# Kernel optimization log

Measured on AMD Instinct MI355X. Metric: run time of the kernel, lower is better.

Reference implementation:

```python
import jax, jax.numpy as jnp
import numpy as np

D_MODEL = 1024
N_HEADS = 16
ORDER = 6          # P
P2 = 2 * ORDER - 1 # 11 collapsed Chebyshev terms
EPS_CLAMP = 1e-6
EPS_DEN = 1e-7


def _beta_np():
    # alpha_j = (j+1)^{-1.5}, j = 0..P-1
    j = np.arange(ORDER, dtype=np.float32)
    alpha = (j + 1.0) ** (-1.5)
    tail = np.flip(np.cumsum(np.flip(alpha)))  # tail[i] = sum_{j>=i} alpha_j
    beta = np.concatenate([np.zeros(1, np.float32), tail[1:].astype(np.float32), np.zeros(ORDER - 1, np.float32)])
    return beta / beta.sum()


def _cheb(x):
    T = [jnp.ones_like(x), x]
    for _ in range(2, P2):
        T.append(2.0 * x * T[-1] - T[-2])
    return jnp.stack(T, axis=3)


def setup_inputs() -> dict:
    key = jax.random.key(0)
    k1, k2, k3 = jax.random.split(key, 3)
    B, S, D = 2, 1024, D_MODEL
    x = jax.random.normal(k1, (B, S, D), dtype=jnp.float32)
    W_in = jax.random.normal(k2, (3 * D, D), dtype=jnp.float32) * 0.02
    W_out = jax.random.normal(k3, (D, D), dtype=jnp.float32) * 0.02
    return {"x": x, "W_in": W_in, "W_out": W_out}


def reference(x, W_in, W_out):
    B, S, D = x.shape
    H, Dh = N_HEADS, D // N_HEADS

    # fused QKV projection (Linear, no bias): y = x @ W_in^T
    qkv = jnp.einsum('bsd,ed->bse', x, W_in)
    q, k, v = jnp.split(qkv, 3, axis=-1)
    # (B,S,H,Dh) -> (B,H,S,Dh)
    q = q.reshape(B, S, H, Dh).transpose(0, 2, 1, 3)
    k = k.reshape(B, S, H, Dh).transpose(0, 2, 1, 3)
    v = v.reshape(B, S, H, Dh).transpose(0, 2, 1, 3)

    inv_sqrt_d = 1.0 / jnp.sqrt(jnp.float32(Dh))
    xq = jnp.clip(q * inv_sqrt_d, -1.0 + EPS_CLAMP, 1.0 - EPS_CLAMP)
    xk = jnp.clip(k * inv_sqrt_d, -1.0 + EPS_CLAMP, 1.0 - EPS_CLAMP)

    Tq = _cheb(xq)  # (B,H,S,P2,Dh)
    Tk = _cheb(xk)  # (B,H,S,P2,Dh)

    beta = jnp.asarray(_beta_np())  # (P2,), same for all heads (fixed buffer)

    # causal prefix sums over sequence dim
    Tv = Tk * v[:, :, :, None, :]             # (B,H,S,P2,Dh)
    kv_prefix = jnp.cumsum(Tv, axis=2)        # (B,H,S,P2,Dh)
    ks_prefix = jnp.cumsum(Tk.sum(axis=-1), axis=2)  # (B,H,S,P2)

    kv_beta = kv_prefix * beta[None, None, None, :, None]
    k_beta = ks_prefix * beta[None, None, None, :]

    num = (Tq * kv_beta).sum(axis=3)                 # (B,H,S,Dh)
    den = (Tq.sum(axis=-1) * k_beta).sum(axis=3)     # (B,H,S)   den_normalization='none'

    out_h = num / (den[..., None] + EPS_DEN)
    out = out_h.transpose(0, 2, 1, 3).reshape(B, S, H * Dh)
    return jnp.einsum('bsd,ed->bse', out, W_out)
```

## Files before the change

kernel.cpp:

```cpp
#include <hip/hip_runtime.h>
#include <hip/hip_bf16.h>
#include <cstddef>
#include <cstdint>

#define BATCH 2
#define SEQ   1024
#define DMODEL 1024
#define NHEADS 16
#define DHEAD 64
#define E3D   3072
#define NCHUNK 64
#define CHUNK 16

#define BETA1 0.45736626f
#define BETA2 0.26218724f
#define BETA3 0.15594524f
#define BETA4 0.08693904f
#define BETA5 0.03756222f

#define RSCALE 2048.f
#define RINV   4.8828125e-4f

typedef __attribute__((ext_vector_type(8))) _Float16 half8;
typedef __attribute__((ext_vector_type(16))) float floatx16;

__device__ __forceinline__ void cp16(const void* g, void* l) {
    __builtin_amdgcn_global_load_lds(
        (const __attribute__((address_space(1))) void*)(uintptr_t)g,
        (__attribute__((address_space(3))) void*)(uintptr_t)l,
        16, 0, 0);
}

__device__ __forceinline__ void split2(float x, unsigned short* H, unsigned short* M) {
    _Float16 h = (_Float16)x;
    float r = (x - (float)h) * RSCALE;
    _Float16 m = (_Float16)r;
    *H = __builtin_bit_cast(unsigned short, h);
    *M = __builtin_bit_cast(unsigned short, m);
}

__device__ __forceinline__ void split2x4(const float4 v,
                                         unsigned short* h, unsigned short* m,
                                         size_t i4) {
    float vv[4] = {v.x, v.y, v.z, v.w};
    unsigned short hh[4], mm[4];
#pragma unroll
    for (int j = 0; j < 4; j++) split2(vv[j], &hh[j], &mm[j]);
    ((ushort4*)h)[i4] = make_ushort4(hh[0], hh[1], hh[2], hh[3]);
    ((ushort4*)m)[i4] = make_ushort4(mm[0], mm[1], mm[2], mm[3]);
}

__device__ __forceinline__ void cheb5(float x, float T[6]) {
    T[0] = 1.f; T[1] = x;
    float tx2 = 2.f * x;
    T[2] = tx2 * T[1] - T[0];
    T[3] = tx2 * T[2] - T[1];
    T[4] = tx2 * T[3] - T[2];
    T[5] = tx2 * T[4] - T[3];
}

__device__ __forceinline__ float clampx(float v) {
    return fminf(fmaxf(v * 0.125f, -1.f + 1e-6f), 1.f - 1e-6f);
}

__device__ __forceinline__ float wave_sum(float x) {
#pragma unroll
    for (int m = 32; m >= 1; m >>= 1) x += __shfl_xor(x, m, 64);
    return x;
}

__global__ __launch_bounds__(256) void k_splitall(
    const float* __restrict__ x, const float* __restrict__ Win,
    unsigned short* __restrict__ Xh, unsigned short* __restrict__ Xm,
    unsigned short* __restrict__ Wh, unsigned short* __restrict__ Wm)
{
    const float* in; unsigned short *h, *m; int i;
    if (blockIdx.x < 2048) {
        in = x; h = Xh; m = Xm;
        i = blockIdx.x * 256 + threadIdx.x;
    } else {
        in = Win; h = Wh; m = Wm;
        i = (blockIdx.x - 2048) * 256 + threadIdx.x;
    }
    split2x4(((const float4*)in)[i], h, m, i);
}

template<int TN>
__global__ __launch_bounds__(256, 2) void gemm_w32(
    const unsigned short* __restrict__ Ah, const unsigned short* __restrict__ Am,
    const unsigned short* __restrict__ Bh, const unsigned short* __restrict__ Bm,
    float* __restrict__ C, int M, int N, int K)
{
    constexpr int NT  = TN / 64;
    constexpr int ASZ = 64 * 32;
    constexpr int BSZ = TN * 32;
    __shared__ unsigned short lds[2 * ASZ + 2 * BSZ];

    const int tid  = threadIdx.x;
    const int w    = tid >> 6;
    const int lane = tid & 63;
    const int m0 = blockIdx.y * 64;
    const int n0 = blockIdx.x * TN;

    const int arow = w * 16 + (lane >> 2);
    const int asg  = (lane & 3) ^ ((arow >> 1) & 3);
    const size_t offA = (size_t)(m0 + arow) * K + asg * 8;
    const int ldsA = (w * 16) * 32;
    size_t offB[NT];
    int ldsB[NT];
#pragma unroll
    for (int j = 0; j < NT; j++) {
        const int brow = j * 64 + w * 16 + (lane >> 2);
        const int bsg  = (lane & 3) ^ ((brow >> 1) & 3);
        offB[j] = (size_t)(n0 + brow) * K + bsg * 8;
        ldsB[j] = (j * 64 + w * 16) * 32;
    }

    const int l32 = lane & 31, q32 = lane >> 5;
    const int wm = w & 1, wn = w >> 1;
    const int ra = wm * 32 + l32;
    const int abase = ra * 32, aswz = (ra >> 1) & 3;
    int bbase[NT], bswz[NT];
#pragma unroll
    for (int nt = 0; nt < NT; nt++) {
        const int rb = wn * (TN / 2) + nt * 32 + l32;
        bbase[nt] = rb * 32;
        bswz[nt] = (rb >> 1) & 3;
    }

    floatx16 acc1[NT] = {};
    floatx16 acc2[NT] = {};

    for (int k0 = 0; k0 < K; k0 += 32) {
        __syncthreads();
        cp16(Ah + offA + k0, &lds[ldsA]);
        cp16(Am + offA + k0, &lds[ASZ + ldsA]);
#pragma unroll
        for (int j = 0; j < NT; j++) {
            cp16(Bh + offB[j] + k0, &lds[2 * ASZ + ldsB[j]]);
            cp16(Bm + offB[j] + k0, &lds[2 * ASZ + BSZ + ldsB[j]]);
        }
        __syncthreads();

#pragma unroll
        for (int kk = 0; kk < 2; kk++) {
            const int ksel = kk * 2 + q32;
            half8 fah = *(const half8*)&lds[abase + ((ksel ^ aswz) * 8)];
            half8 fam = *(const half8*)&lds[ASZ + abase + ((ksel ^ aswz) * 8)];
            half8 fbh[NT], fbm[NT];
#pragma unroll
            for (int nt = 0; nt < NT; nt++) {
                fbh[nt] = *(const half8*)&lds[2 * ASZ + bbase[nt] + ((ksel ^ bswz[nt]) * 8)];
                fbm[nt] = *(const half8*)&lds[2 * ASZ + BSZ + bbase[nt] + ((ksel ^ bswz[nt]) * 8)];
            }
#pragma unroll
            for (int nt = 0; nt < NT; nt++) {
                acc1[nt] = __builtin_amdgcn_mfma_f32_32x32x16_f16(fah, fbh[nt], acc1[nt], 0, 0, 0);
                acc2[nt] = __builtin_amdgcn_mfma_f32_32x32x16_f16(fah, fbm[nt], acc2[nt], 0, 0, 0);
                acc2[nt] = __builtin_amdgcn_mfma_f32_32x32x16_f16(fam, fbh[nt], acc2[nt], 0, 0, 0);
            }
        }
    }

    const int r0 = m0 + wm * 32 + q32 * 4;
#pragma unroll
    for (int nt = 0; nt < NT; nt++) {
        const int c0 = n0 + wn * (TN / 2) + nt * 32 + l32;
#pragma unroll
        for (int reg = 0; reg < 16; reg++) {
            const int row = r0 + (reg & 3) + 8 * (reg >> 2);
            C[(size_t)row * N + c0] = acc1[nt][reg] + acc2[nt][reg] * RINV;
        }
    }
}

__global__ __launch_bounds__(256) void k_mid(
    const float* __restrict__ Wout,
    unsigned short* __restrict__ Wouth, unsigned short* __restrict__ Woutm,
    const float* __restrict__ qkv,
    float* __restrict__ SQB, float* __restrict__ SK, float* __restrict__ KVC)
{
    const int blk = blockIdx.x;
    if (blk < 1024) {
        int i = blk * 256 + threadIdx.x;
        split2x4(((const float4*)Wout)[i], Wouth, Woutm, i);
        return;
    }
    if (blk < 9216) {
        const int lane = threadIdx.x & 63;
        const int pos  = (blk - 1024) * 4 + (threadIdx.x >> 6);
        const int bh = pos >> 10, s = pos & 1023;
        const int b = bh >> 4, h = bh & 15;
        const float* base = qkv + (size_t)(b * SEQ + s) * E3D + h * DHEAD + lane;
        float xq = clampx(base[0]);
        float xk = clampx(base[1024]);
        float Tq[6], Tk[6];
        cheb5(xq, Tq); cheb5(xk, Tk);
        const float BETA[5] = {BETA1, BETA2, BETA3, BETA4, BETA5};
#pragma unroll
        for (int p = 1; p <= 5; p++) {
            float sq = wave_sum(Tq[p]);
            float sk = wave_sum(Tk[p]);
            if (lane == 0) {
                SQB[(size_t)pos * 5 + p - 1] = sq * BETA[p - 1];
                SK[(size_t)pos * 5 + p - 1]  = sk;
            }
        }
        return;
    }
    {
        const int lane = threadIdx.x & 63;
        const int cid = (blk - 9216) * 4 + (threadIdx.x >> 6);
        const int bh = cid >> 6, chunk = cid & 63;
        const int b = bh >> 4, h = bh & 15;
        const float* kb = qkv + (size_t)(b * SEQ + chunk * CHUNK) * E3D + 1024 + h * DHEAD + lane;
        float kv[5] = {0.f, 0.f, 0.f, 0.f, 0.f};
#pragma unroll
        for (int i = 0; i < CHUNK; i++) {
            const float* row = kb + (size_t)i * E3D;
            float xk = clampx(row[0]);
            float v = row[1024];
            float T[6]; cheb5(xk, T);
#pragma unroll
            for (int p = 1; p <= 5; p++) kv[p - 1] += T[p] * v;
        }
#pragma unroll
        for (int p = 0; p < 5; p++) KVC[((size_t)cid * 5 + p) * 64 + lane] = kv[p];
    }
}

__global__ __launch_bounds__(320) void k_prefix(float* __restrict__ KVC,
                                                const float* __restrict__ SK,
                                                float* __restrict__ SKP)
{
    __shared__ float csum[NCHUNK * 5];
    const int bh = blockIdx.x;
    const int t = threadIdx.x;
    float v[NCHUNK];
    const size_t base = (size_t)bh * NCHUNK * 320 + t;
#pragma unroll
    for (int c = 0; c < NCHUNK; c++) v[c] = KVC[base + (size_t)c * 320];
    float run = 0.f;
#pragma unroll
    for (int c = 0; c < NCHUNK; c++) {
        KVC[base + (size_t)c * 320] = run;
        run += v[c];
    }
    {
        const int chunk = t / 5, p = t % 5;
        const float* sb = SK + ((size_t)bh * SEQ + chunk * CHUNK) * 5 + p;
        float s = 0.f;
#pragma unroll
        for (int i = 0; i < CHUNK; i++) s += sb[i * 5];
        csum[chunk * 5 + p] = s;
    }
    __syncthreads();
    if (t < 5) {
        float run2 = 0.f;
        for (int c = 0; c < NCHUNK; c++) {
            SKP[((size_t)bh * NCHUNK + c) * 5 + t] = run2;
            run2 += csum[c * 5 + t];
        }
    }
}

__global__ __launch_bounds__(256) void k_out(const float* __restrict__ qkv,
                                             const float* __restrict__ KVC,
                                             const float* __restrict__ SK,
                                             const float* __restrict__ SKP,
                                             const float* __restrict__ SQB,
                                             unsigned short* __restrict__ OH,
                                             unsigned short* __restrict__ OM)
{
    const int lane = threadIdx.x & 63;
    const int cid = blockIdx.x * 4 + (threadIdx.x >> 6);
    const int bh = cid >> 6, chunk = cid & 63;
    const int b = bh >> 4, h = bh & 15;
    const float BETA[5] = {BETA1, BETA2, BETA3, BETA4, BETA5};

    const int li = lane & 15;
    const int pos = bh * SEQ + chunk * CHUNK + li;
    float den_r = 0.f;
#pragma unroll
    for (int p = 0; p < 5; p++) {
        float v = SK[(size_t)pos * 5 + p];
#pragma unroll
        for (int off = 1; off < 16; off <<= 1) {
            float n = __shfl_up(v, off, 64);
            if (li >= off) v += n;
        }
        den_r += SQB[(size_t)pos * 5 + p] * (SKP[((size_t)bh * NCHUNK + chunk) * 5 + p] + v);
    }

    float kv[5];
#pragma unroll
    for (int p = 0; p < 5; p++) kv[p] = KVC[((size_t)cid * 5 + p) * 64 + lane];

    const float* qb = qkv + (size_t)(b * SEQ + chunk * CHUNK) * E3D + h * DHEAD + lane;
    size_t obase = (size_t)(b * SEQ + chunk * CHUNK) * DMODEL + h * DHEAD + lane;
#pragma unroll
    for (int i = 0; i < CHUNK; i++) {
        const float* row = qb + (size_t)i * E3D;
        float xq = clampx(row[0]);
        float xk = clampx(row[1024]);
        float v = row[2048];
        float Tk_[6]; cheb5(xk, Tk_);
#pragma unroll
        for (int p = 1; p <= 5; p++) kv[p - 1] += Tk_[p] * v;
        float Tq_[6]; cheb5(xq, Tq_);
        float num = 0.f;
#pragma unroll
        for (int p = 1; p <= 5; p++) num += BETA[p - 1] * Tq_[p] * kv[p - 1];
        float d = __shfl(den_r, i, 64);
        float val = num / (d + 1e-7f);
        unsigned short hh, mm;
        split2(val, &hh, &mm);
        size_t oi = obase + (size_t)i * DMODEL;
        OH[oi] = hh; OM[oi] = mm;
    }
}


extern "C" void kernel_launch(void* const* d_in, const int* in_sizes, int n_in,
                              void* d_out, int out_size, void* d_ws, size_t ws_size,
                              hipStream_t stream)
{
    const float* x    = (const float*)d_in[0];
    const float* Win  = (const float*)d_in[1];
    const float* Wout = (const float*)d_in[2];
    float* out = (float*)d_out;
    char* ws = (char*)d_ws;

    float* QKV = (float*)(ws + 0);
    unsigned short* Xh   = (unsigned short*)(ws + 25165824);
    unsigned short* Xm   = (unsigned short*)(ws + 29360128);
    unsigned short* Winh = (unsigned short*)(ws + 33554432);
    unsigned short* Winm = (unsigned short*)(ws + 39845888);
    float* SQB = (float*)(ws + 25165824);
    float* SK  = (float*)(ws + 25821184);
    float* SKP = (float*)(ws + 26476544);
    float* KVC = (float*)(ws + 26517504);
    unsigned short* OHh   = (unsigned short*)(ws + 33554432);
    unsigned short* OHm   = (unsigned short*)(ws + 37748736);
    unsigned short* Wouth = (unsigned short*)(ws + 41943040);
    unsigned short* Woutm = (unsigned short*)(ws + 44040192);

    k_splitall<<<5120, 256, 0, stream>>>(x, Win, Xh, Xm, Winh, Winm);

    gemm_w32<192><<<dim3(16, 32), 256, 0, stream>>>(Xh, Xm, Winh, Winm,
                                                    QKV, BATCH * SEQ, E3D, DMODEL);

    k_mid<<<9728, 256, 0, stream>>>(Wout, Wouth, Woutm, QKV, SQB, SK, KVC);

    k_prefix<<<BATCH * NHEADS, 320, 0, stream>>>(KVC, SK, SKP);

    k_out<<<512, 256, 0, stream>>>(QKV, KVC, SK, SKP, SQB, OHh, OHm);

    gemm_w32<64><<<dim3(16, 32), 256, 0, stream>>>(OHh, OHm, Wouth, Woutm,
                                                   out, BATCH * SEQ, DMODEL, DMODEL);
}
```

Measured before the change: 179.7 us.

## Rework GEMM LDS layout to lane-contiguous fragments and retile QKV projection

Replaces the XOR-swizzled LDS tile layout with a layout where each MFMA fragment is stored contiguously per lane. Fragment reads become simple stride-16 byte loads, and global-to-LDS copies are redistributed evenly across waves. The QKV GEMM tile narrows from 192 to 128 columns with a 24x32 grid, and occupancy hints rise from 2 to 3 blocks per CU. This aims to cut LDS bank conflicts and address arithmetic and to improve wave balance and occupancy. The risk is more register pressure under the tighter launch bound and lower reuse from the smaller tile.

```diff
diff --git a/kernel.cpp b/kernel.cpp
--- a/kernel.cpp
+++ b/kernel.cpp
@@ -86,15 +86,17 @@
 }
 
 template<int TN>
-__global__ __launch_bounds__(256, 2) void gemm_w32(
+__device__ __forceinline__ void gemm_body(
     const unsigned short* __restrict__ Ah, const unsigned short* __restrict__ Am,
     const unsigned short* __restrict__ Bh, const unsigned short* __restrict__ Bm,
     float* __restrict__ C, int M, int N, int K)
 {
-    constexpr int NT  = TN / 64;
-    constexpr int ASZ = 64 * 32;
-    constexpr int BSZ = TN * 32;
-    __shared__ unsigned short lds[2 * ASZ + 2 * BSZ];
+    constexpr int NT     = TN / 64;
+    constexpr int ABYTES = 4096;
+    constexpr int BBYTES = TN * 64;
+    constexpr int NC     = 8 + TN / 8;
+    constexpr int PW     = NC / 4;
+    __shared__ unsigned char lds[2 * ABYTES + 2 * BBYTES];
 
     const int tid  = threadIdx.x;
     const int w    = tid >> 6;
@@ -102,56 +104,52 @@
     const int m0 = blockIdx.y * 64;
     const int n0 = blockIdx.x * TN;
 
-    const int arow = w * 16 + (lane >> 2);
-    const int asg  = (lane & 3) ^ ((arow >> 1) & 3);
-    const size_t offA = (size_t)(m0 + arow) * K + asg * 8;
-    const int ldsA = (w * 16) * 32;
-    size_t offB[NT];
-    int ldsB[NT];
-#pragma unroll
-    for (int j = 0; j < NT; j++) {
-        const int brow = j * 64 + w * 16 + (lane >> 2);
-        const int bsg  = (lane & 3) ^ ((brow >> 1) & 3);
-        offB[j] = (size_t)(n0 + brow) * K + bsg * 8;
-        ldsB[j] = (j * 64 + w * 16) * 32;
-    }
-
-    const int l32 = lane & 31, q32 = lane >> 5;
+    const int lrow = lane & 31;
+    const int lseg = lane >> 5;
+    const unsigned short* src[PW];
+    size_t goff[PW];
+    int loff[PW];
+#pragma unroll
+    for (int j = 0; j < PW; j++) {
+        const int id = w * PW + j;
+        if (id < 8) {
+            const int split = id >> 2, rem = id & 3, gg = rem >> 1, p = rem & 1;
+            src[j]  = split ? Am : Ah;
+            goff[j] = (size_t)(m0 + gg * 32 + lrow) * K + (2 * p + lseg) * 8;
+            loff[j] = split * ABYTES + gg * 2048 + p * 1024;
+        } else {
+            const int bid = id - 8;
+            const int split = bid / (TN / 16), rem = bid % (TN / 16);
+            const int gg = rem >> 1, p = rem & 1;
+            src[j]  = split ? Bm : Bh;
+            goff[j] = (size_t)(n0 + gg * 32 + lrow) * K + (2 * p + lseg) * 8;
+            loff[j] = 2 * ABYTES + split * BBYTES + gg * 2048 + p * 1024;
+        }
+    }
+
     const int wm = w & 1, wn = w >> 1;
-    const int ra = wm * 32 + l32;
-    const int abase = ra * 32, aswz = (ra >> 1) & 3;
-    int bbase[NT], bswz[NT];
-#pragma unroll
-    for (int nt = 0; nt < NT; nt++) {
-        const int rb = wn * (TN / 2) + nt * 32 + l32;
-        bbase[nt] = rb * 32;
-        bswz[nt] = (rb >> 1) & 3;
-    }
+    const int abase  = wm * 2048 + lane * 16;
+    const int bbase0 = 2 * ABYTES + wn * NT * 2048 + lane * 16;
 
     floatx16 acc1[NT] = {};
     floatx16 acc2[NT] = {};
 
     for (int k0 = 0; k0 < K; k0 += 32) {
         __syncthreads();
-        cp16(Ah + offA + k0, &lds[ldsA]);
-        cp16(Am + offA + k0, &lds[ASZ + ldsA]);
-#pragma unroll
-        for (int j = 0; j < NT; j++) {
-            cp16(Bh + offB[j] + k0, &lds[2 * ASZ + ldsB[j]]);
-            cp16(Bm + offB[j] + k0, &lds[2 * ASZ + BSZ + ldsB[j]]);
-        }
+#pragma unroll
+        for (int j = 0; j < PW; j++)
+            cp16(src[j] + goff[j] + k0, &lds[loff[j]]);
         __syncthreads();
 
 #pragma unroll
         for (int kk = 0; kk < 2; kk++) {
-            const int ksel = kk * 2 + q32;
-            half8 fah = *(const half8*)&lds[abase + ((ksel ^ aswz) * 8)];
-            half8 fam = *(const half8*)&lds[ASZ + abase + ((ksel ^ aswz) * 8)];
+            half8 fah = *(const half8*)&lds[abase + kk * 1024];
+            half8 fam = *(const half8*)&lds[ABYTES + abase + kk * 1024];
             half8 fbh[NT], fbm[NT];
 #pragma unroll
             for (int nt = 0; nt < NT; nt++) {
-                fbh[nt] = *(const half8*)&lds[2 * ASZ + bbase[nt] + ((ksel ^ bswz[nt]) * 8)];
-                fbm[nt] = *(const half8*)&lds[2 * ASZ + BSZ + bbase[nt] + ((ksel ^ bswz[nt]) * 8)];
+                fbh[nt] = *(const half8*)&lds[bbase0 + nt * 2048 + kk * 1024];
+                fbm[nt] = *(const half8*)&lds[bbase0 + BBYTES + nt * 2048 + kk * 1024];
             }
 #pragma unroll
             for (int nt = 0; nt < NT; nt++) {
@@ -162,6 +160,7 @@
         }
     }
 
+    const int l32 = lane & 31, q32 = lane >> 5;
     const int r0 = m0 + wm * 32 + q32 * 4;
 #pragma unroll
     for (int nt = 0; nt < NT; nt++) {
@@ -172,6 +171,22 @@
             C[(size_t)row * N + c0] = acc1[nt][reg] + acc2[nt][reg] * RINV;
         }
     }
+}
+
+__global__ __launch_bounds__(256, 3) void gemm1(
+    const unsigned short* __restrict__ Ah, const unsigned short* __restrict__ Am,
+    const unsigned short* __restrict__ Bh, const unsigned short* __restrict__ Bm,
+    float* __restrict__ C, int M, int N, int K)
+{
+    gemm_body<128>(Ah, Am, Bh, Bm, C, M, N, K);
+}
+
+__global__ __launch_bounds__(256, 3) void gemm2(
+    const unsigned short* __restrict__ Ah, const unsigned short* __restrict__ Am,
+    const unsigned short* __restrict__ Bh, const unsigned short* __restrict__ Bm,
+    float* __restrict__ C, int M, int N, int K)
+{
+    gemm_body<64>(Ah, Am, Bh, Bm, C, M, N, K);
 }
 
 __global__ __launch_bounds__(256) void k_mid(
@@ -347,8 +362,8 @@
 
     k_splitall<<<5120, 256, 0, stream>>>(x, Win, Xh, Xm, Winh, Winm);
 
-    gemm_w32<192><<<dim3(16, 32), 256, 0, stream>>>(Xh, Xm, Winh, Winm,
-                                                    QKV, BATCH * SEQ, E3D, DMODEL);
+    gemm1<<<dim3(24, 32), 256, 0, stream>>>(Xh, Xm, Winh, Winm,
+                                            QKV, BATCH * SEQ, E3D, DMODEL);
 
     k_mid<<<9728, 256, 0, stream>>>(Wout, Wouth, Woutm, QKV, SQB, SK, KVC);
 
@@ -356,6 +371,6 @@
 
     k_out<<<512, 256, 0, stream>>>(QKV, KVC, SK, SKP, SQB, OHh, OHm);
 
-    gemm_w32<64><<<dim3(16, 32), 256, 0, stream>>>(OHh, OHm, Wouth, Woutm,
-                                                   out, BATCH * SEQ, DMODEL, DMODEL);
-}
+    gemm2<<<dim3(16, 32), 256, 0, stream>>>(OHh, OHm, Wouth, Woutm,
+                                            out, BATCH * SEQ, DMODEL, DMODEL);
+}
```

Result: slower. 219.8 us (+22.4%).

## Double-buffer split-fp16 GEMM LDS tiles and switch to 16x16x32 MFMA

Applied to the files above, without the earlier changes.

Rewrites the split-precision GEMM kernel so it double-buffers its LDS tiles: the next K-slice is prefetched with global_load_lds while the current one is consumed, which leaves one barrier per iteration instead of two. The MFMA shape moves from 32x32x16 to 16x16x32 with a 2D MT×NT accumulator grid and a generic load-work distribution across waves. The QKV GEMM tile changes to 128x96, and the output GEMM uses 64x64. The cost is twice the LDS footprint and more accumulator registers, which may lower occupancy.

```diff
diff --git a/kernel.cpp b/kernel.cpp
--- a/kernel.cpp
+++ b/kernel.cpp
@@ -22,7 +22,7 @@
 #define RINV   4.8828125e-4f
 
 typedef __attribute__((ext_vector_type(8))) _Float16 half8;
-typedef __attribute__((ext_vector_type(16))) float floatx16;
+typedef __attribute__((ext_vector_type(4))) float floatx4;
 
 __device__ __forceinline__ void cp16(const void* g, void* l) {
     __builtin_amdgcn_global_load_lds(
@@ -85,91 +85,115 @@
     split2x4(((const float4*)in)[i], h, m, i);
 }
 
-template<int TN>
-__global__ __launch_bounds__(256, 2) void gemm_w32(
+template<int TM, int TN>
+__global__ __launch_bounds__(256, 2) void gemm_db(
     const unsigned short* __restrict__ Ah, const unsigned short* __restrict__ Am,
     const unsigned short* __restrict__ Bh, const unsigned short* __restrict__ Bm,
     float* __restrict__ C, int M, int N, int K)
 {
-    constexpr int NT  = TN / 64;
-    constexpr int ASZ = 64 * 32;
-    constexpr int BSZ = TN * 32;
-    __shared__ unsigned short lds[2 * ASZ + 2 * BSZ];
-
-    const int tid  = threadIdx.x;
-    const int w    = tid >> 6;
-    const int lane = tid & 63;
-    const int m0 = blockIdx.y * 64;
-    const int n0 = blockIdx.x * TN;
-
-    const int arow = w * 16 + (lane >> 2);
-    const int asg  = (lane & 3) ^ ((arow >> 1) & 3);
-    const size_t offA = (size_t)(m0 + arow) * K + asg * 8;
-    const int ldsA = (w * 16) * 32;
-    size_t offB[NT];
-    int ldsB[NT];
-#pragma unroll
-    for (int j = 0; j < NT; j++) {
-        const int brow = j * 64 + w * 16 + (lane >> 2);
-        const int bsg  = (lane & 3) ^ ((brow >> 1) & 3);
-        offB[j] = (size_t)(n0 + brow) * K + bsg * 8;
-        ldsB[j] = (j * 64 + w * 16) * 32;
-    }
-
-    const int l32 = lane & 31, q32 = lane >> 5;
+    constexpr int MT = TM / 32;
+    constexpr int NT = TN / 32;
+    constexpr int ABYTES = TM * 64;
+    constexpr int BBYTES = TN * 64;
+    constexpr int BUF = 2 * ABYTES + 2 * BBYTES;
+    constexpr int NC = (2 * TM + 2 * TN) / 16;
+    constexpr int PW = NC / 4;
+    __shared__ unsigned char lds[2 * BUF];
+
+    const int tid = threadIdx.x;
+    const int w = tid >> 6, lane = tid & 63;
+    const int m0 = blockIdx.y * TM, n0 = blockIdx.x * TN;
+
+    const unsigned short* srcp[PW];
+    int goff[PW];
+    int loff[PW];
+    {
+        const int lrow4 = lane >> 2, spos = lane & 3;
+#pragma unroll
+        for (int j = 0; j < PW; j++) {
+            const int id = w * PW + j;
+            if (id < 2 * (TM / 16)) {
+                const int split = id / (TM / 16), g = id % (TM / 16);
+                const int row = g * 16 + lrow4;
+                const int gseg = spos ^ ((row >> 1) & 3);
+                srcp[j] = split ? Am : Ah;
+                goff[j] = (m0 + row) * K + gseg * 8;
+                loff[j] = split * ABYTES + g * 1024;
+            } else {
+                const int id2 = id - 2 * (TM / 16);
+                const int split = id2 / (TN / 16), g = id2 % (TN / 16);
+                const int row = g * 16 + lrow4;
+                const int gseg = spos ^ ((row >> 1) & 3);
+                srcp[j] = split ? Bm : Bh;
+                goff[j] = (n0 + row) * K + gseg * 8;
+                loff[j] = 2 * ABYTES + split * BBYTES + g * 1024;
+            }
+        }
+    }
+
     const int wm = w & 1, wn = w >> 1;
-    const int ra = wm * 32 + l32;
-    const int abase = ra * 32, aswz = (ra >> 1) & 3;
-    int bbase[NT], bswz[NT];
+    const int l16 = lane & 15, q = lane >> 4;
+    int aoff[MT], boff[NT];
+#pragma unroll
+    for (int mt = 0; mt < MT; mt++) {
+        const int r = wm * (TM / 2) + mt * 16 + l16;
+        aoff[mt] = r * 64 + ((q ^ ((r >> 1) & 3)) * 16);
+    }
 #pragma unroll
     for (int nt = 0; nt < NT; nt++) {
-        const int rb = wn * (TN / 2) + nt * 32 + l32;
-        bbase[nt] = rb * 32;
-        bswz[nt] = (rb >> 1) & 3;
-    }
-
-    floatx16 acc1[NT] = {};
-    floatx16 acc2[NT] = {};
+        const int r = wn * (TN / 2) + nt * 16 + l16;
+        boff[nt] = 2 * ABYTES + r * 64 + ((q ^ ((r >> 1) & 3)) * 16);
+    }
+
+    floatx4 acc1[MT][NT] = {};
+    floatx4 acc2[MT][NT] = {};
+
+#pragma unroll
+    for (int j = 0; j < PW; j++)
+        cp16(srcp[j] + goff[j], &lds[loff[j]]);
+    __syncthreads();
 
     for (int k0 = 0; k0 < K; k0 += 32) {
+        const int cur = (k0 >> 5) & 1;
+        if (k0 + 32 < K) {
+            const int nb = (cur ^ 1) * BUF;
+#pragma unroll
+            for (int j = 0; j < PW; j++)
+                cp16(srcp[j] + goff[j] + k0 + 32, &lds[nb + loff[j]]);
+        }
+        const unsigned char* base = &lds[cur * BUF];
+        half8 fbh[NT], fbm[NT];
+#pragma unroll
+        for (int nt = 0; nt < NT; nt++) {
+            fbh[nt] = *(const half8*)(base + boff[nt]);
+            fbm[nt] = *(const half8*)(base + BBYTES + boff[nt]);
+        }
+#pragma unroll
+        for (int mt = 0; mt < MT; mt++) {
+            half8 fah = *(const half8*)(base + aoff[mt]);
+            half8 fam = *(const half8*)(base + ABYTES + aoff[mt]);
+#pragma unroll
+            for (int nt = 0; nt < NT; nt++) {
+                acc1[mt][nt] = __builtin_amdgcn_mfma_f32_16x16x32_f16(
+                    fah, fbh[nt], acc1[mt][nt], 0, 0, 0);
+                acc2[mt][nt] = __builtin_amdgcn_mfma_f32_16x16x32_f16(
+                    fah, fbm[nt], acc2[mt][nt], 0, 0, 0);
+                acc2[mt][nt] = __builtin_amdgcn_mfma_f32_16x16x32_f16(
+                    fam, fbh[nt], acc2[mt][nt], 0, 0, 0);
+            }
+        }
         __syncthreads();
-        cp16(Ah + offA + k0, &lds[ldsA]);
-        cp16(Am + offA + k0, &lds[ASZ + ldsA]);
-#pragma unroll
-        for (int j = 0; j < NT; j++) {
-            cp16(Bh + offB[j] + k0, &lds[2 * ASZ + ldsB[j]]);
-            cp16(Bm + offB[j] + k0, &lds[2 * ASZ + BSZ + ldsB[j]]);
-        }
-        __syncthreads();
-
-#pragma unroll
-        for (int kk = 0; kk < 2; kk++) {
-            const int ksel = kk * 2 + q32;
-            half8 fah = *(const half8*)&lds[abase + ((ksel ^ aswz) * 8)];
-            half8 fam = *(const half8*)&lds[ASZ + abase + ((ksel ^ aswz) * 8)];
-            half8 fbh[NT], fbm[NT];
-#pragma unroll
-            for (int nt = 0; nt < NT; nt++) {
-                fbh[nt] = *(const half8*)&lds[2 * ASZ + bbase[nt] + ((ksel ^ bswz[nt]) * 8)];
-                fbm[nt] = *(const half8*)&lds[2 * ASZ + BSZ + bbase[nt] + ((ksel ^ bswz[nt]) * 8)];
-            }
-#pragma unroll
-            for (int nt = 0; nt < NT; nt++) {
-                acc1[nt] = __builtin_amdgcn_mfma_f32_32x32x16_f16(fah, fbh[nt], acc1[nt], 0, 0, 0);
-                acc2[nt] = __builtin_amdgcn_mfma_f32_32x32x16_f16(fah, fbm[nt], acc2[nt], 0, 0, 0);
-                acc2[nt] = __builtin_amdgcn_mfma_f32_32x32x16_f16(fam, fbh[nt], acc2[nt], 0, 0, 0);
-            }
-        }
-    }
-
-    const int r0 = m0 + wm * 32 + q32 * 4;
-#pragma unroll
-    for (int nt = 0; nt < NT; nt++) {
-        const int c0 = n0 + wn * (TN / 2) + nt * 32 + l32;
-#pragma unroll
-        for (int reg = 0; reg < 16; reg++) {
-            const int row = r0 + (reg & 3) + 8 * (reg >> 2);
-            C[(size_t)row * N + c0] = acc1[nt][reg] + acc2[nt][reg] * RINV;
+    }
+
+#pragma unroll
+    for (int mt = 0; mt < MT; mt++) {
+        const int row0 = m0 + wm * (TM / 2) + mt * 16 + q * 4;
+#pragma unroll
+        for (int nt = 0; nt < NT; nt++) {
+            const int col = n0 + wn * (TN / 2) + nt * 16 + l16;
+#pragma unroll
+            for (int r = 0; r < 4; r++)
+                C[(size_t)(row0 + r) * N + col] = acc1[mt][nt][r] + acc2[mt][nt][r] * RINV;
         }
     }
 }
@@ -347,8 +371,8 @@
 
     k_splitall<<<5120, 256, 0, stream>>>(x, Win, Xh, Xm, Winh, Winm);
 
-    gemm_w32<192><<<dim3(16, 32), 256, 0, stream>>>(Xh, Xm, Winh, Winm,
-                                                    QKV, BATCH * SEQ, E3D, DMODEL);
+    gemm_db<128, 96><<<dim3(32, 16), 256, 0, stream>>>(Xh, Xm, Winh, Winm,
+                                                       QKV, BATCH * SEQ, E3D, DMODEL);
 
     k_mid<<<9728, 256, 0, stream>>>(Wout, Wouth, Woutm, QKV, SQB, SK, KVC);
 
@@ -356,6 +380,6 @@
 
     k_out<<<512, 256, 0, stream>>>(QKV, KVC, SK, SKP, SQB, OHh, OHm);
 
-    gemm_w32<64><<<dim3(16, 32), 256, 0, stream>>>(OHh, OHm, Wouth, Woutm,
-                                                   out, BATCH * SEQ, DMODEL, DMODEL);
-}
+    gemm_db<64, 64><<<dim3(16, 32), 256, 0, stream>>>(OHh, OHm, Wouth, Woutm,
+                                                      out, BATCH * SEQ, DMODEL, DMODEL);
+}
```

New measurement: 169.9 us (median of 2 runs). -5.4%, faster.
